# Kernel optimization log

Hardware: AMD Instinct MI355X
Metric: run time of the kernel (lower is better)

## Reference

```python
import jax, jax.numpy as jnp
import numpy as np

B, S, H = 4, 2048, 768
NUM_HEADS = 12
HEAD_DIM = H // NUM_HEADS


def setup_inputs() -> dict:
    key = jax.random.key(0)
    k1, k2, k3 = jax.random.split(key, 3)
    hidden_states = jax.random.normal(k1, (B, S, H), dtype=jnp.float32)
    # torch Linear weight [out,in]; store transposed [in,out] for x @ W
    w_qkv = jax.random.normal(k2, (H, 3 * H), dtype=jnp.float32) * (1.0 / np.sqrt(H))
    w_out = jax.random.normal(k3, (H, H), dtype=jnp.float32) * (1.0 / np.sqrt(H))
    return {"hidden_states": hidden_states, "w_qkv": w_qkv, "w_out": w_out}


def reference(hidden_states, w_qkv, w_out):
    b, s, h = hidden_states.shape
    qkv = hidden_states @ w_qkv                      # [b,s,3h]
    qkv = qkv.reshape(b, s, 3, NUM_HEADS, HEAD_DIM)
    qkv = jnp.transpose(qkv, (2, 0, 3, 1, 4))        # [3,b,nh,s,hd]
    q, k, v = qkv[0], qkv[1], qkv[2]
    scale = 1.0 / np.sqrt(HEAD_DIM).astype(np.float32)
    scores = jnp.einsum('bhqd,bhkd->bhqk', q, k) * scale   # [b,nh,s,s]
    causal = jnp.triu(jnp.ones((s, s), dtype=bool), k=1)
    scores = jnp.where(causal, jnp.float32(-jnp.inf), scores)
    attn = jax.nn.softmax(scores, axis=-1)
    # dropout is identity in eval mode
    out = jnp.einsum('bhqk,bhkd->bhqd', attn, v)      # [b,nh,s,hd]
    out = jnp.transpose(out, (0, 2, 1, 3)).reshape(b, s, h)
    return out @ w_out
```

## Files before the change

### kernel.cpp

```cpp
#include <hip/hip_runtime.h>
#include <stdint.h>

#define B_ 4
#define S_ 2048
#define H_ 768
#define NH_ 12
#define HD_ 64
#define BH_ (B_ * NH_)

#define QSCALE 0.18033688011112042f

typedef __attribute__((ext_vector_type(4))) float f32x4;
typedef __attribute__((ext_vector_type(16))) float f32x16;
typedef __attribute__((ext_vector_type(8))) __bf16 bf16x8;
typedef __attribute__((ext_vector_type(8))) unsigned short ushort8;
typedef __attribute__((ext_vector_type(2))) unsigned int u32x2;
typedef __attribute__((ext_vector_type(4))) unsigned int u32x4;

__device__ __forceinline__ unsigned short bf16rne(float f) {
  union { float f; unsigned int u; } v;
  v.f = f;
  unsigned int u = v.u;
  return (unsigned short)((u + 0x7fffu + ((u >> 16) & 1u)) >> 16);
}

#if __has_builtin(__builtin_amdgcn_cvt_pk_bf16_f32)
__device__ __forceinline__ unsigned int pk2(float a, float b) {
  auto r = __builtin_amdgcn_cvt_pk_bf16_f32(a, b);
  return *(unsigned int*)&r;
}
#else
__device__ __forceinline__ unsigned int pk2(float a, float b) {
  return (unsigned int)bf16rne(a) | ((unsigned int)bf16rne(b) << 16);
}
#endif

#if __has_builtin(__builtin_amdgcn_exp2f)
#define EXP2F(x) __builtin_amdgcn_exp2f(x)
#else
#define EXP2F(x) exp2f(x)
#endif

#if __has_builtin(__builtin_amdgcn_permlane32_swap)
__device__ __forceinline__ u32x2 permswap(unsigned a, unsigned b) {
  u32x2 r = __builtin_amdgcn_permlane32_swap(a, b, false, false);
  return r;
}
#else
__device__ __forceinline__ u32x2 permswap(unsigned a, unsigned b) {
  int l = (int)(threadIdx.x & 63);
  unsigned ap = (unsigned)__shfl((int)a, l ^ 32, 64);
  unsigned bp = (unsigned)__shfl((int)b, l ^ 32, 64);
  u32x2 r;
  r[0] = (l & 32) ? bp : a;
  r[1] = (l & 32) ? b : ap;
  return r;
}
#endif

__device__ __forceinline__ void gll16(const void* g, void* l) {
  __builtin_amdgcn_global_load_lds(
      (const __attribute__((address_space(1))) unsigned int*)g,
      (__attribute__((address_space(3))) unsigned int*)l, 16, 0, 0);
}

__device__ __forceinline__ void tconv_body(const float* __restrict__ in,
                                           unsigned short* __restrict__ out,
                                           int R, int C, int bx, int by,
                                           unsigned short (*tile)[72], int tid) {
  int c0 = bx * 64, r0 = by * 64;
#pragma unroll
  for (int i = 0; i < 4; ++i) {
    int c = i * 256 + tid;
    int row = c >> 4, col4 = (c & 15) * 4;
    float4 v = *(const float4*)(in + (size_t)(r0 + row) * C + c0 + col4);
    *(uint2*)(&tile[row][col4]) = (uint2){pk2(v.x, v.y), pk2(v.z, v.w)};
  }
  __syncthreads();
#pragma unroll
  for (int i = 0; i < 2; ++i) {
    int c = i * 256 + tid;
    int oc = c >> 3, r8 = (c & 7) * 8;
    ushort8 v;
#pragma unroll
    for (int j = 0; j < 8; ++j) v[j] = tile[r8 + j][oc];
    *(ushort8*)(out + (size_t)(c0 + oc) * R + r0 + r8) = v;
  }
}

__global__ __launch_bounds__(256) void prep_kernel(const float* __restrict__ hs,
                                                   const float* __restrict__ wqkv,
                                                   const float* __restrict__ wout,
                                                   unsigned short* __restrict__ Xbf,
                                                   unsigned short* __restrict__ Wqkvt,
                                                   unsigned short* __restrict__ Woutt) {
  __shared__ unsigned short tile[64][72];
  int bid = blockIdx.x, tid = threadIdx.x;
  if (bid < 3072) {
    int i = (bid * 256 + tid) * 8;
    const float4* p = (const float4*)(hs + i);
    float4 a = p[0], b = p[1];
    uint4 r = {pk2(a.x, a.y), pk2(a.z, a.w), pk2(b.x, b.y), pk2(b.z, b.w)};
    *(uint4*)(Xbf + i) = r;
  } else if (bid < 3504) {
    int idx = bid - 3072;
    tconv_body(wqkv, Wqkvt, 768, 2304, idx % 36, idx / 36, tile, tid);
  } else {
    int idx = bid - 3504;
    tconv_body(wout, Woutt, 768, 768, idx % 12, idx / 12, tile, tid);
  }
}

template <int MODE>
__device__ __forceinline__ void gemm_core(const unsigned short* __restrict__ A,
                                          const unsigned short* __restrict__ Bm,
                                          void* __restrict__ Cout, int N, int K,
                                          int bm, int bn,
                                          unsigned short* As, unsigned short* Bs) {
  int tid = threadIdx.x;
  int lane = tid & 63, wave = tid >> 6;
  int quad = lane >> 4, l16 = lane & 15;
  int wm = (wave & 1) * 64, wn = (wave >> 1) * 64;
  const unsigned short* Ag = A + (size_t)bm * 128 * K;
  const unsigned short* Bg = Bm + (size_t)bn * 128 * K;

  f32x4 zero = {0.f, 0.f, 0.f, 0.f};
  f32x4 acc[4][4];
#pragma unroll
  for (int mt = 0; mt < 4; ++mt)
#pragma unroll
    for (int nt = 0; nt < 4; ++nt) acc[mt][nt] = zero;

  for (int k0 = 0; k0 < K; k0 += 32) {
#pragma unroll
    for (int i = 0; i < 2; ++i) {
      int c = i * 256 + tid;
      int row = c >> 2, off = (c & 3) * 8;
      gll16(Ag + (size_t)row * K + k0 + off, As + c * 8);
      gll16(Bg + (size_t)row * K + k0 + off, Bs + c * 8);
    }
    __syncthreads();
    bf16x8 af[4], bf[4];
#pragma unroll
    for (int mt = 0; mt < 4; ++mt)
      af[mt] = *(const bf16x8*)(As + (wm + mt * 16 + l16) * 32 + quad * 8);
#pragma unroll
    for (int nt = 0; nt < 4; ++nt)
      bf[nt] = *(const bf16x8*)(Bs + (wn + nt * 16 + l16) * 32 + quad * 8);
#pragma unroll
    for (int mt = 0; mt < 4; ++mt)
#pragma unroll
      for (int nt = 0; nt < 4; ++nt) {
        if (MODE == 2)
          acc[mt][nt] = __builtin_amdgcn_mfma_f32_16x16x32_bf16(af[mt], bf[nt], acc[mt][nt], 0, 0, 0);
        else
          acc[mt][nt] = __builtin_amdgcn_mfma_f32_16x16x32_bf16(bf[nt], af[mt], acc[mt][nt], 0, 0, 0);
      }
    __syncthreads();
  }

  if (MODE == 0) {
    unsigned short* qkv = (unsigned short*)Cout;
    int which = (bn >= 6);
#pragma unroll
    for (int mt = 0; mt < 4; ++mt)
#pragma unroll
      for (int nt = 0; nt < 4; ++nt) {
        int f0 = bn * 128 + wn + nt * 16 + quad * 4;
        int tm = bm * 128 + wm + mt * 16 + l16;
        int rem = f0 - which * 768;
        int head = rem >> 6, d0 = rem & 63;
        int b = tm >> 11, s = tm & 2047;
        if (which == 0) {
          uint2 pkv = {pk2(acc[mt][nt][0] * QSCALE, acc[mt][nt][1] * QSCALE),
                       pk2(acc[mt][nt][2] * QSCALE, acc[mt][nt][3] * QSCALE)};
          *(uint2*)(qkv + (((size_t)b * NH_ + head) * S_ + s) * HD_ + d0) = pkv;
        } else {
          uint2 pkv = {pk2(acc[mt][nt][0], acc[mt][nt][1]),
                       pk2(acc[mt][nt][2], acc[mt][nt][3])};
          int t = s >> 6, kb = (s >> 5) & 1, row = s & 31;
          int dk = d0 >> 4, hh = (d0 >> 3) & 1, off = d0 & 7;
          *(uint2*)(qkv + ((size_t)(BH_ + b * NH_ + head)) * S_ * HD_ + t * 4096
                    + ((kb * 4 + dk) * 64 + hh * 32 + row) * 8 + off) = pkv;
        }
      }
  } else {
    unsigned short* vt = (unsigned short*)Cout;
#pragma unroll
    for (int mt = 0; mt < 4; ++mt)
#pragma unroll
      for (int nt = 0; nt < 4; ++nt) {
        int f = bn * 128 + wn + nt * 16 + l16;
        int t0 = bm * 128 + wm + mt * 16 + quad * 4;
        int rem = f - 1536;
        int head = rem >> 6, d = rem & 63;
        int b = t0 >> 11, s0 = t0 & 2047;
        int tile = s0 >> 6, sin = s0 & 63;
        int ks = sin >> 4, hh = (sin >> 3) & 1, off = sin & 7;
        int db = d >> 5, drow = d & 31;
        uint2 pkv = {pk2(acc[mt][nt][0], acc[mt][nt][1]),
                     pk2(acc[mt][nt][2], acc[mt][nt][3])};
        *(uint2*)(vt + ((size_t)(b * NH_ + head)) * HD_ * S_ + tile * 4096
                  + ((db * 4 + ks) * 64 + hh * 32 + drow) * 8 + off) = pkv;
      }
  }
}

__global__ __launch_bounds__(256) void gemm_qkv(const unsigned short* __restrict__ A,
                                                const unsigned short* __restrict__ Bm,
                                                unsigned short* __restrict__ QK,
                                                unsigned short* __restrict__ Vt) {
  __shared__ unsigned short As[128 * 32];
  __shared__ unsigned short Bs[128 * 32];
  int bm = blockIdx.x, bn = blockIdx.y;
  if (bn < 12)
    gemm_core<0>(A, Bm, QK, 2304, 768, bm, bn, As, Bs);
  else
    gemm_core<2>(A, Bm, Vt, 2304, 768, bm, bn, As, Bs);
}

__global__ __launch_bounds__(256) void gemm_out64(const unsigned short* __restrict__ A,
                                                  const unsigned short* __restrict__ Bm,
                                                  float* __restrict__ Cout) {
  __shared__ unsigned short As[64 * 32];
  __shared__ unsigned short Bs[128 * 32];
  const int K = 768, N = 768;
  int bm = blockIdx.x, bn = blockIdx.y;
  int tid = threadIdx.x, lane = tid & 63, wave = tid >> 6;
  int quad = lane >> 4, l16 = lane & 15;
  int wn = wave * 32;
  const unsigned short* Ag = A + (size_t)bm * 64 * K;
  const unsigned short* Bg = Bm + (size_t)bn * 128 * K;

  f32x4 zero = {0.f, 0.f, 0.f, 0.f};
  f32x4 acc[4][2];
#pragma unroll
  for (int mt = 0; mt < 4; ++mt)
#pragma unroll
    for (int nt = 0; nt < 2; ++nt) acc[mt][nt] = zero;

  for (int k0 = 0; k0 < K; k0 += 32) {
    {
      int row = tid >> 2, off = (tid & 3) * 8;
      gll16(Ag + (size_t)row * K + k0 + off, As + tid * 8);
    }
#pragma unroll
    for (int i = 0; i < 2; ++i) {
      int c = i * 256 + tid;
      int row = c >> 2, off = (c & 3) * 8;
      gll16(Bg + (size_t)row * K + k0 + off, Bs + c * 8);
    }
    __syncthreads();
    bf16x8 af[4], bf[2];
#pragma unroll
    for (int mt = 0; mt < 4; ++mt)
      af[mt] = *(const bf16x8*)(As + (mt * 16 + l16) * 32 + quad * 8);
#pragma unroll
    for (int nt = 0; nt < 2; ++nt)
      bf[nt] = *(const bf16x8*)(Bs + (wn + nt * 16 + l16) * 32 + quad * 8);
#pragma unroll
    for (int mt = 0; mt < 4; ++mt)
#pragma unroll
      for (int nt = 0; nt < 2; ++nt)
        acc[mt][nt] = __builtin_amdgcn_mfma_f32_16x16x32_bf16(bf[nt], af[mt], acc[mt][nt], 0, 0, 0);
    __syncthreads();
  }

#pragma unroll
  for (int mt = 0; mt < 4; ++mt)
#pragma unroll
    for (int nt = 0; nt < 2; ++nt) {
      int f0 = bn * 128 + wn + nt * 16 + quad * 4;
      int tm = bm * 64 + mt * 16 + l16;
      *(f32x4*)(Cout + (size_t)tm * N + f0) = acc[mt][nt];
    }
}

__global__ __launch_bounds__(256, 3) void attn_kernel(const unsigned short* __restrict__ Q,
                                                      const unsigned short* __restrict__ Kg,
                                                      const unsigned short* __restrict__ Vt,
                                                      unsigned short* __restrict__ O) {
  __shared__ unsigned short Ks[3][64 * 64];
  __shared__ unsigned short Vs[3][64 * 64];
  const int pi_[16] = {0, 1, 3, 5, 7, 9, 11, 13, 15, 14, 12, 10, 8, 6, 4, 2};
  int bh = blockIdx.x;
  int y = blockIdx.y;
  int qt = pi_[(bh + y) & 15];
  int tid = threadIdx.x, lane = tid & 63, wave = tid >> 6;
  int l32 = lane & 31, h = lane >> 5;
  const unsigned short* Qp = Q + (size_t)bh * S_ * HD_;
  int q0 = qt * 128;
  int qrow = q0 + wave * 32 + l32;
  int kmax_w = (q0 + wave * 32 + 31) >> 6;
  int kmax_b = 2 * qt + 1;

  const unsigned short* kS = Kg + (size_t)bh * S_ * HD_;
  const unsigned short* vS = Vt + (size_t)bh * HD_ * S_;

  auto stage = [&](int t, int buf) {
#pragma unroll
    for (int i = 0; i < 2; ++i) {
      int c = (i * 256 + tid) * 8;
      gll16(kS + (size_t)t * 4096 + c, &Ks[buf][c]);
      gll16(vS + (size_t)t * 4096 + c, &Vs[buf][c]);
    }
  };

  bf16x8 qf[4];
#pragma unroll
  for (int dk = 0; dk < 4; ++dk)
    qf[dk] = *(const bf16x8*)(Qp + (size_t)qrow * HD_ + dk * 16 + h * 8);

  stage(0, 0);
  stage(1, 1);

  bf16x8 ones;
#pragma unroll
  for (int j = 0; j < 8; ++j) ones[j] = (__bf16)1.0f;

  const int flin = lane * 8;

  f32x16 zero16;
#pragma unroll
  for (int j = 0; j < 16; ++j) zero16[j] = 0.f;
  f32x16 o[2], rsv;
  o[0] = zero16; o[1] = zero16; rsv = zero16;

  auto body = [&](int t, const unsigned short* Kb, const unsigned short* Vb) {
    f32x16 sf[2];
    sf[0] = zero16; sf[1] = zero16;
#pragma unroll
    for (int kb = 0; kb < 2; ++kb)
#pragma unroll
      for (int dk = 0; dk < 4; ++dk) {
        bf16x8 kf = *(const bf16x8*)(Kb + (kb * 4 + dk) * 512 + flin);
        sf[kb] = __builtin_amdgcn_mfma_f32_32x32x16_bf16(kf, qf[dk], sf[kb], 0, 0, 0);
      }

    if (t == kmax_w) {
#pragma unroll
      for (int kb = 0; kb < 2; ++kb)
#pragma unroll
        for (int r = 0; r < 16; ++r)
          if (t * 64 + kb * 32 + (r & 3) + 8 * (r >> 2) + 4 * h > qrow) sf[kb][r] = -1e30f;
    }

    unsigned p01[8], p23[8];
#pragma unroll
    for (int kb = 0; kb < 2; ++kb)
#pragma unroll
      for (int g = 0; g < 4; ++g) {
        p01[kb * 4 + g] = pk2(EXP2F(sf[kb][g * 4 + 0]), EXP2F(sf[kb][g * 4 + 1]));
        p23[kb * 4 + g] = pk2(EXP2F(sf[kb][g * 4 + 2]), EXP2F(sf[kb][g * 4 + 3]));
      }

#pragma unroll
    for (int ks = 0; ks < 4; ++ks) {
      u32x2 a02 = permswap(p01[2 * ks], p01[2 * ks + 1]);
      u32x2 a13 = permswap(p23[2 * ks], p23[2 * ks + 1]);
      u32x4 pu;
      pu[0] = a02[0]; pu[1] = a13[0]; pu[2] = a02[1]; pu[3] = a13[1];
      bf16x8 pf = *(bf16x8*)&pu;
      rsv = __builtin_amdgcn_mfma_f32_32x32x16_bf16(ones, pf, rsv, 0, 0, 0);
#pragma unroll
      for (int db = 0; db < 2; ++db) {
        bf16x8 vf = *(const bf16x8*)(Vb + (db * 4 + ks) * 512 + flin);
        o[db] = __builtin_amdgcn_mfma_f32_32x32x16_bf16(vf, pf, o[db], 0, 0, 0);
      }
    }
  };

  int buf = 0;
  for (int t = 0; t <= kmax_b; ++t) {
    if (t < kmax_b)
      asm volatile("s_waitcnt vmcnt(4)" ::: "memory");
    else
      asm volatile("s_waitcnt vmcnt(0)" ::: "memory");
    __builtin_amdgcn_s_barrier();
    int nb = buf + 2; if (nb >= 3) nb -= 3;
    if (t + 2 <= kmax_b) stage(t + 2, nb);
    if (t <= kmax_w) body(t, &Ks[buf][0], &Vs[buf][0]);
    ++buf; if (buf == 3) buf = 0;
  }

  float inv = 1.f / rsv[0];
  int b = bh / NH_, hh = bh % NH_;
#pragma unroll
  for (int db = 0; db < 2; ++db)
#pragma unroll
    for (int g = 0; g < 4; ++g) {
      uint2 pkv = {pk2(o[db][g * 4 + 0] * inv, o[db][g * 4 + 1] * inv),
                   pk2(o[db][g * 4 + 2] * inv, o[db][g * 4 + 3] * inv)};
      int d0 = db * 32 + 8 * g + 4 * h;
      *(uint2*)(O + ((size_t)b * S_ + qrow) * H_ + hh * HD_ + d0) = pkv;
    }
}

extern "C" void kernel_launch(void* const* d_in, const int* in_sizes, int n_in,
                              void* d_out, int out_size, void* d_ws, size_t ws_size,
                              hipStream_t stream) {
  (void)in_sizes; (void)n_in; (void)out_size; (void)ws_size;
  const float* hs = (const float*)d_in[0];
  const float* wqkv = (const float*)d_in[1];
  const float* wout = (const float*)d_in[2];
  float* out = (float*)d_out;

  unsigned short* Xbf = (unsigned short*)d_ws;
  unsigned short* Wqkvt = Xbf + (size_t)8192 * 768;
  unsigned short* Woutt = Wqkvt + (size_t)2304 * 768;
  unsigned short* QK = Woutt + (size_t)768 * 768;
  unsigned short* Vt = QK + (size_t)2 * BH_ * S_ * HD_;
  unsigned short* Attn = Xbf;

  prep_kernel<<<3648, 256, 0, stream>>>(hs, wqkv, wout, Xbf, Wqkvt, Woutt);
  gemm_qkv<<<dim3(64, 18), 256, 0, stream>>>(Xbf, Wqkvt, QK, Vt);
  attn_kernel<<<dim3(48, 16), 256, 0, stream>>>(QK, QK + (size_t)BH_ * S_ * HD_, Vt, Attn);
  gemm_out64<<<dim3(128, 6), 256, 0, stream>>>(Attn, Woutt, out);
}
```

Before: 193.4 us.

## Triple-buffer GEMM LDS staging with swizzled layout and single barrier

Both the QKV and output-projection GEMMs now use a three-stage LDS ring. Global-to-LDS loads run two k-steps ahead, and each step waits with an explicit vmcnt count and a single s_barrier instead of two __syncthreads. The LDS tile is also XOR-swizzled on the 16-byte chunk index, applied to the source address and the fragment reads, to reduce bank conflicts. This hides global load latency behind MFMA work, but triples the GEMM shared memory, which may lower occupancy.

```diff
diff --git a/kernel.cpp b/kernel.cpp
--- a/kernel.cpp
+++ b/kernel.cpp
@@ -124,6 +124,31 @@
   const unsigned short* Ag = A + (size_t)bm * 128 * K;
   const unsigned short* Bg = Bm + (size_t)bn * 128 * K;
 
+  int so[2];
+#pragma unroll
+  for (int i = 0; i < 2; ++i) {
+    int c = i * 256 + tid;
+    int row = c >> 2;
+    so[i] = row * K + (((c & 3) ^ ((row >> 1) & 3)) << 3);
+  }
+  auto stage = [&](int s, int b3) {
+    unsigned short* Ad = As + b3 * 4096;
+    unsigned short* Bd = Bs + b3 * 4096;
+#pragma unroll
+    for (int i = 0; i < 2; ++i) {
+      int c = i * 256 + tid;
+      gll16(Ag + so[i] + s * 32, Ad + c * 8);
+      gll16(Bg + so[i] + s * 32, Bd + c * 8);
+    }
+  };
+
+  int rp = (quad ^ ((l16 >> 1) & 3)) * 8;
+  int aoff[4], boff[4];
+#pragma unroll
+  for (int mt = 0; mt < 4; ++mt) aoff[mt] = (wm + mt * 16 + l16) * 32 + rp;
+#pragma unroll
+  for (int nt = 0; nt < 4; ++nt) boff[nt] = (wn + nt * 16 + l16) * 32 + rp;
+
   f32x4 zero = {0.f, 0.f, 0.f, 0.f};
   f32x4 acc[4][4];
 #pragma unroll
@@ -131,22 +156,25 @@
 #pragma unroll
     for (int nt = 0; nt < 4; ++nt) acc[mt][nt] = zero;
 
-  for (int k0 = 0; k0 < K; k0 += 32) {
-#pragma unroll
-    for (int i = 0; i < 2; ++i) {
-      int c = i * 256 + tid;
-      int row = c >> 2, off = (c & 3) * 8;
-      gll16(Ag + (size_t)row * K + k0 + off, As + c * 8);
-      gll16(Bg + (size_t)row * K + k0 + off, Bs + c * 8);
-    }
-    __syncthreads();
+  int ns = K >> 5;
+  stage(0, 0);
+  stage(1, 1);
+  int buf = 0;
+  for (int s = 0; s < ns; ++s) {
+    if (s < ns - 1)
+      asm volatile("s_waitcnt vmcnt(4)" ::: "memory");
+    else
+      asm volatile("s_waitcnt vmcnt(0)" ::: "memory");
+    __builtin_amdgcn_s_barrier();
+    int nb = buf + 2; if (nb >= 3) nb -= 3;
+    if (s + 2 < ns) stage(s + 2, nb);
+    const unsigned short* Ab = As + buf * 4096;
+    const unsigned short* Bb = Bs + buf * 4096;
     bf16x8 af[4], bf[4];
 #pragma unroll
-    for (int mt = 0; mt < 4; ++mt)
-      af[mt] = *(const bf16x8*)(As + (wm + mt * 16 + l16) * 32 + quad * 8);
-#pragma unroll
-    for (int nt = 0; nt < 4; ++nt)
-      bf[nt] = *(const bf16x8*)(Bs + (wn + nt * 16 + l16) * 32 + quad * 8);
+    for (int mt = 0; mt < 4; ++mt) af[mt] = *(const bf16x8*)(Ab + aoff[mt]);
+#pragma unroll
+    for (int nt = 0; nt < 4; ++nt) bf[nt] = *(const bf16x8*)(Bb + boff[nt]);
 #pragma unroll
     for (int mt = 0; mt < 4; ++mt)
 #pragma unroll
@@ -156,7 +184,7 @@
         else
           acc[mt][nt] = __builtin_amdgcn_mfma_f32_16x16x32_bf16(bf[nt], af[mt], acc[mt][nt], 0, 0, 0);
       }
-    __syncthreads();
+    ++buf; if (buf == 3) buf = 0;
   }
 
   if (MODE == 0) {
@@ -210,8 +238,8 @@
                                                 const unsigned short* __restrict__ Bm,
                                                 unsigned short* __restrict__ QK,
                                                 unsigned short* __restrict__ Vt) {
-  __shared__ unsigned short As[128 * 32];
-  __shared__ unsigned short Bs[128 * 32];
+  __shared__ unsigned short As[3 * 128 * 32];
+  __shared__ unsigned short Bs[3 * 128 * 32];
   int bm = blockIdx.x, bn = blockIdx.y;
   if (bn < 12)
     gemm_core<0>(A, Bm, QK, 2304, 768, bm, bn, As, Bs);
@@ -222,8 +250,8 @@
 __global__ __launch_bounds__(256) void gemm_out64(const unsigned short* __restrict__ A,
                                                   const unsigned short* __restrict__ Bm,
                                                   float* __restrict__ Cout) {
-  __shared__ unsigned short As[64 * 32];
-  __shared__ unsigned short Bs[128 * 32];
+  __shared__ unsigned short As[3 * 64 * 32];
+  __shared__ unsigned short Bs[3 * 128 * 32];
   const int K = 768, N = 768;
   int bm = blockIdx.x, bn = blockIdx.y;
   int tid = threadIdx.x, lane = tid & 63, wave = tid >> 6;
@@ -232,6 +260,29 @@
   const unsigned short* Ag = A + (size_t)bm * 64 * K;
   const unsigned short* Bg = Bm + (size_t)bn * 128 * K;
 
+  int rowA = tid >> 2;
+  int soA = rowA * K + (((tid & 3) ^ ((rowA >> 1) & 3)) << 3);
+  int soB[2];
+#pragma unroll
+  for (int i = 0; i < 2; ++i) {
+    int c = i * 256 + tid;
+    int row = c >> 2;
+    soB[i] = row * K + (((c & 3) ^ ((row >> 1) & 3)) << 3);
+  }
+  auto stage = [&](int s, int b3) {
+    gll16(Ag + soA + s * 32, As + b3 * 2048 + tid * 8);
+#pragma unroll
+    for (int i = 0; i < 2; ++i)
+      gll16(Bg + soB[i] + s * 32, Bs + b3 * 4096 + (i * 256 + tid) * 8);
+  };
+
+  int rp = (quad ^ ((l16 >> 1) & 3)) * 8;
+  int aoff[4], boff[2];
+#pragma unroll
+  for (int mt = 0; mt < 4; ++mt) aoff[mt] = (mt * 16 + l16) * 32 + rp;
+#pragma unroll
+  for (int nt = 0; nt < 2; ++nt) boff[nt] = (wn + nt * 16 + l16) * 32 + rp;
+
   f32x4 zero = {0.f, 0.f, 0.f, 0.f};
   f32x4 acc[4][2];
 #pragma unroll
@@ -239,31 +290,31 @@
 #pragma unroll
     for (int nt = 0; nt < 2; ++nt) acc[mt][nt] = zero;
 
-  for (int k0 = 0; k0 < K; k0 += 32) {
-    {
-      int row = tid >> 2, off = (tid & 3) * 8;
-      gll16(Ag + (size_t)row * K + k0 + off, As + tid * 8);
-    }
-#pragma unroll
-    for (int i = 0; i < 2; ++i) {
-      int c = i * 256 + tid;
-      int row = c >> 2, off = (c & 3) * 8;
-      gll16(Bg + (size_t)row * K + k0 + off, Bs + c * 8);
-    }
-    __syncthreads();
+  int ns = K >> 5;
+  stage(0, 0);
+  stage(1, 1);
+  int buf = 0;
+  for (int s = 0; s < ns; ++s) {
+    if (s < ns - 1)
+      asm volatile("s_waitcnt vmcnt(3)" ::: "memory");
+    else
+      asm volatile("s_waitcnt vmcnt(0)" ::: "memory");
+    __builtin_amdgcn_s_barrier();
+    int nb = buf + 2; if (nb >= 3) nb -= 3;
+    if (s + 2 < ns) stage(s + 2, nb);
+    const unsigned short* Ab = As + buf * 2048;
+    const unsigned short* Bb = Bs + buf * 4096;
     bf16x8 af[4], bf[2];
 #pragma unroll
-    for (int mt = 0; mt < 4; ++mt)
-      af[mt] = *(const bf16x8*)(As + (mt * 16 + l16) * 32 + quad * 8);
-#pragma unroll
-    for (int nt = 0; nt < 2; ++nt)
-      bf[nt] = *(const bf16x8*)(Bs + (wn + nt * 16 + l16) * 32 + quad * 8);
+    for (int mt = 0; mt < 4; ++mt) af[mt] = *(const bf16x8*)(Ab + aoff[mt]);
+#pragma unroll
+    for (int nt = 0; nt < 2; ++nt) bf[nt] = *(const bf16x8*)(Bb + boff[nt]);
 #pragma unroll
     for (int mt = 0; mt < 4; ++mt)
 #pragma unroll
       for (int nt = 0; nt < 2; ++nt)
         acc[mt][nt] = __builtin_amdgcn_mfma_f32_16x16x32_bf16(bf[nt], af[mt], acc[mt][nt], 0, 0, 0);
-    __syncthreads();
+    ++buf; if (buf == 3) buf = 0;
   }
 
 #pragma unroll
```

Result: slower. 211.5 us (+9.4%).

## Double-buffer QKV GEMM LDS tiles with swizzled layout and async prefetch

Applied to the files above, without the earlier changes.

The QKV projection GEMM now keeps two LDS buffers and issues the global-to-LDS loads for the next K-slice before computing the current one, using an explicit vmcnt wait instead of a full sync. Source column offsets are XOR-swizzled by row so the fragment reads from LDS hit fewer bank conflicts. Launch bounds request 5 waves per SIMD. This targets the memory latency exposed by the single-buffered loop, at the cost of doubling LDS per block and raising register pressure.

```diff
diff --git a/kernel.cpp b/kernel.cpp
--- a/kernel.cpp
+++ b/kernel.cpp
@@ -124,6 +124,31 @@
   const unsigned short* Ag = A + (size_t)bm * 128 * K;
   const unsigned short* Bg = Bm + (size_t)bn * 128 * K;
 
+  int so[2];
+#pragma unroll
+  for (int i = 0; i < 2; ++i) {
+    int c = i * 256 + tid;
+    int row = c >> 2;
+    so[i] = row * K + (((c & 3) ^ ((row >> 1) & 3)) << 3);
+  }
+  auto stage = [&](int s, int b2) {
+    unsigned short* Ad = As + b2 * 4096;
+    unsigned short* Bd = Bs + b2 * 4096;
+#pragma unroll
+    for (int i = 0; i < 2; ++i) {
+      int c = i * 256 + tid;
+      gll16(Ag + so[i] + s * 32, Ad + c * 8);
+      gll16(Bg + so[i] + s * 32, Bd + c * 8);
+    }
+  };
+
+  int rp = (quad ^ ((l16 >> 1) & 3)) * 8;
+  int aoff[4], boff[4];
+#pragma unroll
+  for (int mt = 0; mt < 4; ++mt) aoff[mt] = (wm + mt * 16 + l16) * 32 + rp;
+#pragma unroll
+  for (int nt = 0; nt < 4; ++nt) boff[nt] = (wn + nt * 16 + l16) * 32 + rp;
+
   f32x4 zero = {0.f, 0.f, 0.f, 0.f};
   f32x4 acc[4][4];
 #pragma unroll
@@ -131,22 +156,24 @@
 #pragma unroll
     for (int nt = 0; nt < 4; ++nt) acc[mt][nt] = zero;
 
-  for (int k0 = 0; k0 < K; k0 += 32) {
-#pragma unroll
-    for (int i = 0; i < 2; ++i) {
-      int c = i * 256 + tid;
-      int row = c >> 2, off = (c & 3) * 8;
-      gll16(Ag + (size_t)row * K + k0 + off, As + c * 8);
-      gll16(Bg + (size_t)row * K + k0 + off, Bs + c * 8);
-    }
-    __syncthreads();
+  int ns = K >> 5;
+  stage(0, 0);
+  int buf = 0;
+  for (int s = 0; s < ns; ++s) {
+    if (s + 1 < ns) {
+      stage(s + 1, buf ^ 1);
+      asm volatile("s_waitcnt vmcnt(4)" ::: "memory");
+    } else {
+      asm volatile("s_waitcnt vmcnt(0)" ::: "memory");
+    }
+    __builtin_amdgcn_s_barrier();
+    const unsigned short* Ab = As + buf * 4096;
+    const unsigned short* Bb = Bs + buf * 4096;
     bf16x8 af[4], bf[4];
 #pragma unroll
-    for (int mt = 0; mt < 4; ++mt)
-      af[mt] = *(const bf16x8*)(As + (wm + mt * 16 + l16) * 32 + quad * 8);
-#pragma unroll
-    for (int nt = 0; nt < 4; ++nt)
-      bf[nt] = *(const bf16x8*)(Bs + (wn + nt * 16 + l16) * 32 + quad * 8);
+    for (int mt = 0; mt < 4; ++mt) af[mt] = *(const bf16x8*)(Ab + aoff[mt]);
+#pragma unroll
+    for (int nt = 0; nt < 4; ++nt) bf[nt] = *(const bf16x8*)(Bb + boff[nt]);
 #pragma unroll
     for (int mt = 0; mt < 4; ++mt)
 #pragma unroll
@@ -156,7 +183,8 @@
         else
           acc[mt][nt] = __builtin_amdgcn_mfma_f32_16x16x32_bf16(bf[nt], af[mt], acc[mt][nt], 0, 0, 0);
       }
-    __syncthreads();
+    __builtin_amdgcn_s_barrier();
+    buf ^= 1;
   }
 
   if (MODE == 0) {
@@ -206,12 +234,12 @@
   }
 }
 
-__global__ __launch_bounds__(256) void gemm_qkv(const unsigned short* __restrict__ A,
-                                                const unsigned short* __restrict__ Bm,
-                                                unsigned short* __restrict__ QK,
-                                                unsigned short* __restrict__ Vt) {
-  __shared__ unsigned short As[128 * 32];
-  __shared__ unsigned short Bs[128 * 32];
+__global__ __launch_bounds__(256, 5) void gemm_qkv(const unsigned short* __restrict__ A,
+                                                   const unsigned short* __restrict__ Bm,
+                                                   unsigned short* __restrict__ QK,
+                                                   unsigned short* __restrict__ Vt) {
+  __shared__ unsigned short As[2 * 128 * 32];
+  __shared__ unsigned short Bs[2 * 128 * 32];
   int bm = blockIdx.x, bn = blockIdx.y;
   if (bn < 12)
     gemm_core<0>(A, Bm, QK, 2304, 768, bm, bn, As, Bs);
```

New measurement: 210.6 us. +8.9%, slower.
